# Optimization experiments

Hardware: AMD Instinct MI355X
Metric: run time of the kernel (lower is better)

## Reference

```python
import jax, jax.numpy as jnp
import numpy as np

NUM_NEG_PAIRS = 64
NUM_NEG_INDICES_FOR_LOSS = 16
B, C, H, W = 1, 64, 768, 768
HW = H * W


def setup_inputs() -> dict:
    key = jax.random.key(0)
    k1, k2, k3, k4 = jax.random.split(key, 4)
    feats1 = jax.random.normal(k1, (B, C, H, W), dtype=jnp.float32)
    feats2 = jax.random.normal(k2, (B, C, H, W), dtype=jnp.float32)
    positive_pairs = jax.random.randint(k3, (64, 2), 0, HW, dtype=jnp.int64 if jax.config.jax_enable_x64 else jnp.int32)
    negative_indices = jax.random.randint(k4, (NUM_NEG_PAIRS,), 0, HW, dtype=jnp.int64 if jax.config.jax_enable_x64 else jnp.int32)
    return {"feats1": feats1, "feats2": feats2,
            "positive_pairs": positive_pairs,
            "negative_indices": negative_indices}


def reference(feats1, feats2, positive_pairs, negative_indices):
    # feats1/feats2: [1, C, H, W] -> flatten to [C, HW] (matches .view(C, -1) with B=1)
    f1 = feats1.reshape(C, -1)
    f2 = feats2.reshape(C, -1)
    sel = f1[:, negative_indices]                      # [C, P]
    # squared L2 distance of each selected feature vs all HW locations of feats2
    # ||a-b||^2 = ||a||^2 + ||b||^2 - 2 a.b  (ReLU as in original; dist is nonneg)
    d = (jnp.sum(sel * sel, axis=0)[:, None]
         + jnp.sum(f2 * f2, axis=0)[None, :]
         - 2.0 * jnp.einsum('cp,cn->pn', sel, f2))     # [P, HW]
    d = jax.nn.relu(d)
    # NOTE: the original's mask-exclusion check compares FLOAT distance values
    # against an INT index mask (`dist[...].item() in mask`), which is never true
    # for continuous features, so the effective math is: take the K smallest
    # distances per negative, negate, and average.
    smallest = -jax.lax.top_k(-d, NUM_NEG_INDICES_FOR_LOSS)[0]   # [P, K] smallest dists
    negative_loss = jnp.mean(-smallest, axis=1)                   # [P]
    return jnp.mean(negative_loss)
```

## Files before the change

kernel.cpp:

```cpp
#include <hip/hip_runtime.h>
#include <cstdint>

#define CD 64
#define HWD 589824
#define K1_BLOCKS (HWD / 128)
#define FMAXV 3.402823466e+38f

#define AS1 __attribute__((address_space(1)))
#define AS3 __attribute__((address_space(3)))

typedef float f32x16 __attribute__((ext_vector_type(16)));
typedef short bf16x8 __attribute__((ext_vector_type(8)));

__device__ __forceinline__ short f2bf(float f) {
    unsigned u = __float_as_uint(f);
    u = u + 0x7FFFu + ((u >> 16) & 1u);
    return (short)(u >> 16);
}

__device__ __forceinline__ void ins4(float4& t, float x) {
    if (x < t.w) {
        if (x < t.z) { t.w = t.z;
            if (x < t.y) { t.z = t.y;
                if (x < t.x) { t.y = t.x; t.x = x; } else t.y = x;
            } else t.z = x;
        } else t.w = x;
    }
}

__global__ __launch_bounds__(64) void kA_pack(
    const float* __restrict__ f1, const int* __restrict__ nidx,
    short* __restrict__ sel_bf, float* __restrict__ sel2,
    unsigned* __restrict__ ticket)
{
    const int p = blockIdx.x, k = threadIdx.x;
    if (p == 0 && k == 0) *ticket = 0u;
    float v = f1[(long)k * HWD + nidx[p]];
    float s = v * v;
#pragma unroll
    for (int off = 32; off; off >>= 1) s += __shfl_xor(s, off);
    sel_bf[p * CD + k] = f2bf(v);
    if (k == 0) sel2[p] = s;
}

__global__ __launch_bounds__(256, 4) void k1_topk(
    const float* __restrict__ f2, const short* __restrict__ sel_bf,
    const float* __restrict__ sel2, float4* __restrict__ cells)
{
    __shared__ float lds[CD][128];
    __shared__ float4 lm[4][CD];
    const int tid = threadIdx.x;
    const int lane = tid & 63, wid = tid >> 6;
    const int l31 = lane & 31, lh = lane >> 5;
    const long n0 = (long)blockIdx.x * 128;

    {
        const int srow2 = lane >> 5;
        const int scol  = (lane & 31) * 4;
#pragma unroll
        for (int kk = 0; kk < 8; ++kk) {
            int k = wid * 16 + kk * 2;
            const float* gp = f2 + (long)(k + srow2) * HWD + n0 + scol;
            __builtin_amdgcn_global_load_lds((const AS1 void*)gp,
                                             (AS3 void*)&lds[k][0], 16, 0, 0);
        }
    }

    bf16x8 sf0[4], sf1[4];
#pragma unroll
    for (int ks = 0; ks < 4; ++ks) {
        sf0[ks] = *(const bf16x8*)(sel_bf + l31 * CD + 16 * ks + 8 * lh);
        sf1[ks] = *(const bf16x8*)(sel_bf + (l31 + 32) * CD + 16 * ks + 8 * lh);
    }
    const float sel20 = sel2[l31], sel21 = sel2[l31 + 32];

    __syncthreads();

    const int col = wid * 32 + l31;
    float fs = 0.f;
    f32x16 a0, a1;
#pragma unroll
    for (int i = 0; i < 16; ++i) { a0[i] = 0.f; a1[i] = 0.f; }
#pragma unroll
    for (int ks = 0; ks < 4; ++ks) {
        bf16x8 af;
#pragma unroll
        for (int j = 0; j < 8; ++j) {
            float v = lds[16 * ks + 8 * lh + j][col];
            fs += v * v;
            af[j] = f2bf(v);
        }
        a0 = __builtin_amdgcn_mfma_f32_32x32x16_bf16(af, sf0[ks], a0, 0, 0, 0);
        a1 = __builtin_amdgcn_mfma_f32_32x32x16_bf16(af, sf1[ks], a1, 0, 0, 0);
    }
    fs += __shfl_xor(fs, 32);

    float4 t = make_float4(FMAXV, FMAXV, FMAXV, FMAXV);
    float4 u = t;
#pragma unroll
    for (int i = 0; i < 16; ++i) {
        int r = (i & 3) + 8 * (i >> 2) + 4 * lh;
        float fr2 = __shfl(fs, r);
        ins4(t, fmaxf(sel20 + fr2 - 2.f * a0[i], 0.f));
        ins4(u, fmaxf(sel21 + fr2 - 2.f * a1[i], 0.f));
    }

    {
        float4 o;
        o.x = __shfl_xor(t.x, 32); o.y = __shfl_xor(t.y, 32);
        o.z = __shfl_xor(t.z, 32); o.w = __shfl_xor(t.w, 32);
        ins4(t, o.x); ins4(t, o.y); ins4(t, o.z); ins4(t, o.w);
        o.x = __shfl_xor(u.x, 32); o.y = __shfl_xor(u.y, 32);
        o.z = __shfl_xor(u.z, 32); o.w = __shfl_xor(u.w, 32);
        ins4(u, o.x); ins4(u, o.y); ins4(u, o.z); ins4(u, o.w);
    }
    if (lh == 0) { lm[wid][l31] = t; lm[wid][l31 + 32] = u; }
    __syncthreads();

    if (tid < CD) {
        float4 m  = lm[0][tid];
        float4 b1 = lm[1][tid], b2 = lm[2][tid], b3 = lm[3][tid];
        ins4(m, b1.x); ins4(m, b1.y); ins4(m, b1.z); ins4(m, b1.w);
        ins4(m, b2.x); ins4(m, b2.y); ins4(m, b2.z); ins4(m, b2.w);
        ins4(m, b3.x); ins4(m, b3.y); ins4(m, b3.z); ins4(m, b3.w);
        cells[(long)blockIdx.x * CD + tid] = m;
    }
}

__global__ __launch_bounds__(1024) void k2_sel(
    const float4* __restrict__ cells, float* __restrict__ partial,
    unsigned* __restrict__ ticket, float* __restrict__ out)
{
    const int p = blockIdx.x;
    const int tid = threadIdx.x;
    const int lane = tid & 63, wid = tid >> 6;
    __shared__ unsigned long long wmin[16];

    float4 b0 = cells[(long)(tid)        * CD + p];
    float4 b1 = cells[(long)(tid + 1024) * CD + p];
    float4 b2 = cells[(long)(tid + 2048) * CD + p];
    float4 b3 = cells[(long)(tid + 3072) * CD + p];
    float4 b4 = (tid < K1_BLOCKS - 4096)
                ? cells[(long)(tid + 4096) * CD + p]
                : make_float4(FMAXV, FMAXV, FMAXV, FMAXV);

    float4 t = make_float4(FMAXV, FMAXV, FMAXV, FMAXV);
    ins4(t, b0.x); ins4(t, b0.y); ins4(t, b0.z); ins4(t, b0.w);
    ins4(t, b1.x); ins4(t, b1.y); ins4(t, b1.z); ins4(t, b1.w);
    ins4(t, b2.x); ins4(t, b2.y); ins4(t, b2.z); ins4(t, b2.w);
    ins4(t, b3.x); ins4(t, b3.y); ins4(t, b3.z); ins4(t, b3.w);
    ins4(t, b4.x); ins4(t, b4.y); ins4(t, b4.z); ins4(t, b4.w);

    float sum = 0.f;
    for (int rd = 0; rd < 16; ++rd) {
        unsigned long long key =
            ((unsigned long long)__float_as_uint(t.x) << 32) | (unsigned)tid;
#pragma unroll
        for (int off = 32; off; off >>= 1) {
            unsigned long long o = __shfl_xor(key, off);
            if (o < key) key = o;
        }
        if (lane == 0) wmin[wid] = key;
        __syncthreads();
        unsigned long long gk = wmin[0];
#pragma unroll
        for (int w = 1; w < 16; ++w) if (wmin[w] < gk) gk = wmin[w];
        sum += __uint_as_float((unsigned)(gk >> 32));
        if ((unsigned)(gk & 0xFFFFFFFFu) == (unsigned)tid) {
            t.x = t.y; t.y = t.z; t.z = t.w; t.w = FMAXV;
        }
        __syncthreads();
    }

    if (tid == 0) {
        partial[p] = sum;
        __threadfence();
        unsigned tk = atomicAdd(ticket, 1u);
        if (tk == CD - 1) {
            __threadfence();
            float s = 0.f;
            const volatile float* vp = partial;
            for (int q = 0; q < CD; ++q) s += vp[q];
            out[0] = -s / 1024.0f;
        }
    }
}

extern "C" void kernel_launch(void* const* d_in, const int* in_sizes, int n_in,
                              void* d_out, int out_size, void* d_ws, size_t ws_size,
                              hipStream_t stream)
{
    const float* f1   = (const float*)d_in[0];
    const float* f2   = (const float*)d_in[1];
    const int*   nidx = (const int*)d_in[3];
    float* out = (float*)d_out;

    float4*   cells   = (float4*)d_ws;
    short*    sel_bf  = (short*)(cells + (long)K1_BLOCKS * CD);
    float*    sel2    = (float*)(sel_bf + CD * CD);
    float*    partial = sel2 + CD;
    unsigned* ticket  = (unsigned*)(partial + CD);

    kA_pack<<<CD,         64, 0, stream>>>(f1, nidx, sel_bf, sel2, ticket);
    k1_topk<<<K1_BLOCKS, 256, 0, stream>>>(f2, sel_bf, sel2, cells);
    k2_sel <<<CD,       1024, 0, stream>>>(cells, partial, ticket, out);
}
```

Measured before the change: 83.16 us.

## Make k1 persistent over four tiles with double-buffered async LDS loads

The top-k distance kernel now launches 1152 blocks, and each block processes four consecutive 128-column tiles. While the current tile runs its MFMA and insertion work, the next tile's global-to-LDS loads are already in flight in a second buffer, controlled by explicit waitcnt and barriers. This is meant to hide load latency and to amortise the per-block setup and selector register loads. In exchange, LDS use per block doubles, the occupancy hint drops to 2, and correctness depends on the hand-tuned vmcnt count matching the number of outstanding loads.

```diff
diff --git a/kernel.cpp b/kernel.cpp
--- a/kernel.cpp
+++ b/kernel.cpp
@@ -3,7 +3,9 @@
 
 #define CD 64
 #define HWD 589824
-#define K1_BLOCKS (HWD / 128)
+#define K1_GRID 1152
+#define T_PER 4
+#define K1_ROWS (K1_GRID * T_PER)
 #define FMAXV 3.402823466e+38f
 
 #define AS1 __attribute__((address_space(1)))
@@ -43,28 +45,28 @@
     if (k == 0) sel2[p] = s;
 }
 
-__global__ __launch_bounds__(256, 4) void k1_topk(
+__global__ __launch_bounds__(256, 2) void k1_topk(
     const float* __restrict__ f2, const short* __restrict__ sel_bf,
     const float* __restrict__ sel2, float4* __restrict__ cells)
 {
-    __shared__ float lds[CD][128];
+    __shared__ float lds[2][CD][128];
     __shared__ float4 lm[4][CD];
     const int tid = threadIdx.x;
     const int lane = tid & 63, wid = tid >> 6;
     const int l31 = lane & 31, lh = lane >> 5;
-    const long n0 = (long)blockIdx.x * 128;
-
-    {
-        const int srow2 = lane >> 5;
-        const int scol  = (lane & 31) * 4;
-#pragma unroll
-        for (int kk = 0; kk < 8; ++kk) {
-            int k = wid * 16 + kk * 2;
-            const float* gp = f2 + (long)(k + srow2) * HWD + n0 + scol;
-            __builtin_amdgcn_global_load_lds((const AS1 void*)gp,
-                                             (AS3 void*)&lds[k][0], 16, 0, 0);
-        }
-    }
+    const long nb = (long)blockIdx.x * (T_PER * 128);
+
+#define STAGE(buf, ncol0) do {                                              \
+        const int srow2_ = lane >> 5;                                       \
+        const int scol_  = (lane & 31) * 4;                                 \
+        _Pragma("unroll")                                                   \
+        for (int kk = 0; kk < 8; ++kk) {                                    \
+            int k_ = wid * 16 + kk * 2;                                     \
+            const float* gp_ = f2 + (long)(k_ + srow2_) * HWD + (ncol0) + scol_; \
+            __builtin_amdgcn_global_load_lds((const AS1 void*)gp_,          \
+                                             (AS3 void*)&lds[buf][k_][0], 16, 0, 0); \
+        }                                                                   \
+    } while (0)
 
     bf16x8 sf0[4], sf1[4];
 #pragma unroll
@@ -73,58 +75,77 @@
         sf1[ks] = *(const bf16x8*)(sel_bf + (l31 + 32) * CD + 16 * ks + 8 * lh);
     }
     const float sel20 = sel2[l31], sel21 = sel2[l31 + 32];
-
-    __syncthreads();
-
-    const int col = wid * 32 + l31;
-    float fs = 0.f;
-    f32x16 a0, a1;
-#pragma unroll
-    for (int i = 0; i < 16; ++i) { a0[i] = 0.f; a1[i] = 0.f; }
-#pragma unroll
-    for (int ks = 0; ks < 4; ++ks) {
-        bf16x8 af;
-#pragma unroll
-        for (int j = 0; j < 8; ++j) {
-            float v = lds[16 * ks + 8 * lh + j][col];
-            fs += v * v;
-            af[j] = f2bf(v);
-        }
-        a0 = __builtin_amdgcn_mfma_f32_32x32x16_bf16(af, sf0[ks], a0, 0, 0, 0);
-        a1 = __builtin_amdgcn_mfma_f32_32x32x16_bf16(af, sf1[ks], a1, 0, 0, 0);
-    }
-    fs += __shfl_xor(fs, 32);
-
-    float4 t = make_float4(FMAXV, FMAXV, FMAXV, FMAXV);
-    float4 u = t;
-#pragma unroll
-    for (int i = 0; i < 16; ++i) {
-        int r = (i & 3) + 8 * (i >> 2) + 4 * lh;
-        float fr2 = __shfl(fs, r);
-        ins4(t, fmaxf(sel20 + fr2 - 2.f * a0[i], 0.f));
-        ins4(u, fmaxf(sel21 + fr2 - 2.f * a1[i], 0.f));
-    }
-
-    {
-        float4 o;
-        o.x = __shfl_xor(t.x, 32); o.y = __shfl_xor(t.y, 32);
-        o.z = __shfl_xor(t.z, 32); o.w = __shfl_xor(t.w, 32);
-        ins4(t, o.x); ins4(t, o.y); ins4(t, o.z); ins4(t, o.w);
-        o.x = __shfl_xor(u.x, 32); o.y = __shfl_xor(u.y, 32);
-        o.z = __shfl_xor(u.z, 32); o.w = __shfl_xor(u.w, 32);
-        ins4(u, o.x); ins4(u, o.y); ins4(u, o.z); ins4(u, o.w);
-    }
-    if (lh == 0) { lm[wid][l31] = t; lm[wid][l31 + 32] = u; }
-    __syncthreads();
-
-    if (tid < CD) {
-        float4 m  = lm[0][tid];
-        float4 b1 = lm[1][tid], b2 = lm[2][tid], b3 = lm[3][tid];
-        ins4(m, b1.x); ins4(m, b1.y); ins4(m, b1.z); ins4(m, b1.w);
-        ins4(m, b2.x); ins4(m, b2.y); ins4(m, b2.z); ins4(m, b2.w);
-        ins4(m, b3.x); ins4(m, b3.y); ins4(m, b3.z); ins4(m, b3.w);
-        cells[(long)blockIdx.x * CD + tid] = m;
-    }
+    __builtin_amdgcn_sched_barrier(0);
+
+    STAGE(0, nb);
+    __builtin_amdgcn_sched_barrier(0);
+
+#pragma unroll
+    for (int t = 0; t < T_PER; ++t) {
+        if (t + 1 < T_PER) {
+            STAGE((t + 1) & 1, nb + (long)(t + 1) * 128);
+            __builtin_amdgcn_sched_barrier(0);
+            asm volatile("s_waitcnt vmcnt(8)" ::: "memory");
+        } else {
+            asm volatile("s_waitcnt vmcnt(0)" ::: "memory");
+        }
+        __builtin_amdgcn_sched_barrier(0);
+        __builtin_amdgcn_s_barrier();
+        __builtin_amdgcn_sched_barrier(0);
+
+        const int col = wid * 32 + l31;
+        float fs = 0.f;
+        f32x16 a0, a1;
+#pragma unroll
+        for (int i = 0; i < 16; ++i) { a0[i] = 0.f; a1[i] = 0.f; }
+#pragma unroll
+        for (int ks = 0; ks < 4; ++ks) {
+            bf16x8 af;
+#pragma unroll
+            for (int j = 0; j < 8; ++j) {
+                float v = lds[t & 1][16 * ks + 8 * lh + j][col];
+                fs += v * v;
+                af[j] = f2bf(v);
+            }
+            a0 = __builtin_amdgcn_mfma_f32_32x32x16_bf16(af, sf0[ks], a0, 0, 0, 0);
+            a1 = __builtin_amdgcn_mfma_f32_32x32x16_bf16(af, sf1[ks], a1, 0, 0, 0);
+        }
+        fs += __shfl_xor(fs, 32);
+
+        float4 tt = make_float4(FMAXV, FMAXV, FMAXV, FMAXV);
+        float4 uu = tt;
+#pragma unroll
+        for (int i = 0; i < 16; ++i) {
+            int r = (i & 3) + 8 * (i >> 2) + 4 * lh;
+            float fr2 = __shfl(fs, r);
+            ins4(tt, fmaxf(sel20 + fr2 - 2.f * a0[i], 0.f));
+            ins4(uu, fmaxf(sel21 + fr2 - 2.f * a1[i], 0.f));
+        }
+        {
+            float4 o;
+            o.x = __shfl_xor(tt.x, 32); o.y = __shfl_xor(tt.y, 32);
+            o.z = __shfl_xor(tt.z, 32); o.w = __shfl_xor(tt.w, 32);
+            ins4(tt, o.x); ins4(tt, o.y); ins4(tt, o.z); ins4(tt, o.w);
+            o.x = __shfl_xor(uu.x, 32); o.y = __shfl_xor(uu.y, 32);
+            o.z = __shfl_xor(uu.z, 32); o.w = __shfl_xor(uu.w, 32);
+            ins4(uu, o.x); ins4(uu, o.y); ins4(uu, o.z); ins4(uu, o.w);
+        }
+        if (lh == 0) { lm[wid][l31] = tt; lm[wid][l31 + 32] = uu; }
+        asm volatile("s_waitcnt lgkmcnt(0)" ::: "memory");
+        __builtin_amdgcn_sched_barrier(0);
+        __builtin_amdgcn_s_barrier();
+        __builtin_amdgcn_sched_barrier(0);
+
+        if (wid == (t & 3)) {
+            float4 m  = lm[0][lane];
+            float4 b1 = lm[1][lane], b2 = lm[2][lane], b3 = lm[3][lane];
+            ins4(m, b1.x); ins4(m, b1.y); ins4(m, b1.z); ins4(m, b1.w);
+            ins4(m, b2.x); ins4(m, b2.y); ins4(m, b2.z); ins4(m, b2.w);
+            ins4(m, b3.x); ins4(m, b3.y); ins4(m, b3.z); ins4(m, b3.w);
+            cells[(long)(blockIdx.x * T_PER + t) * CD + lane] = m;
+        }
+    }
+#undef STAGE
 }
 
 __global__ __launch_bounds__(1024) void k2_sel(
@@ -140,7 +161,7 @@
     float4 b1 = cells[(long)(tid + 1024) * CD + p];
     float4 b2 = cells[(long)(tid + 2048) * CD + p];
     float4 b3 = cells[(long)(tid + 3072) * CD + p];
-    float4 b4 = (tid < K1_BLOCKS - 4096)
+    float4 b4 = (tid < K1_ROWS - 4096)
                 ? cells[(long)(tid + 4096) * CD + p]
                 : make_float4(FMAXV, FMAXV, FMAXV, FMAXV);
 
@@ -196,12 +217,12 @@
     float* out = (float*)d_out;
 
     float4*   cells   = (float4*)d_ws;
-    short*    sel_bf  = (short*)(cells + (long)K1_BLOCKS * CD);
+    short*    sel_bf  = (short*)(cells + (long)K1_ROWS * CD);
     float*    sel2    = (float*)(sel_bf + CD * CD);
     float*    partial = sel2 + CD;
     unsigned* ticket  = (unsigned*)(partial + CD);
 
-    kA_pack<<<CD,         64, 0, stream>>>(f1, nidx, sel_bf, sel2, ticket);
-    k1_topk<<<K1_BLOCKS, 256, 0, stream>>>(f2, sel_bf, sel2, cells);
-    k2_sel <<<CD,       1024, 0, stream>>>(cells, partial, ticket, out);
-}
+    kA_pack<<<CD,        64, 0, stream>>>(f1, nidx, sel_bf, sel2, ticket);
+    k1_topk<<<K1_GRID,  256, 0, stream>>>(f2, sel_bf, sel2, cells);
+    k2_sel <<<CD,      1024, 0, stream>>>(cells, partial, ticket, out);
+}
```

New measurement: 108.8 us. 30.9% more time.

## Make each wave own four 32-column tiles with per-wave LDS and direct cell output

Applied to the files above, without the earlier changes.

Each wave now handles four consecutive 32-column tiles of feats2, loading every tile into its own per-wave LDS slice and keeping a running top-4 across tiles. This removes the block-level __syncthreads and the cross-wave LDS merge, and amortizes the selection-fragment loads over more work. The grid shrinks to 1152 blocks, and each wave writes its own cell row, so the cell count stays at 4608 for the second kernel. The trade-off is that each tile load is followed by a full vmcnt wait with no prefetch, so memory latency is serialized within a wave. Fewer blocks may also leave fewer waves in flight to hide that latency.

```diff
diff --git a/kernel.cpp b/kernel.cpp
--- a/kernel.cpp
+++ b/kernel.cpp
@@ -3,7 +3,9 @@
 
 #define CD 64
 #define HWD 589824
-#define K1_BLOCKS (HWD / 128)
+#define K1_GRID 1152
+#define T_PER 4
+#define K1_ROWS (K1_GRID * 4)
 #define FMAXV 3.402823466e+38f
 
 #define AS1 __attribute__((address_space(1)))
@@ -47,24 +49,12 @@
     const float* __restrict__ f2, const short* __restrict__ sel_bf,
     const float* __restrict__ sel2, float4* __restrict__ cells)
 {
-    __shared__ float lds[CD][128];
-    __shared__ float4 lm[4][CD];
+    __shared__ float lds[4][CD][32];
     const int tid = threadIdx.x;
     const int lane = tid & 63, wid = tid >> 6;
     const int l31 = lane & 31, lh = lane >> 5;
-    const long n0 = (long)blockIdx.x * 128;
-
-    {
-        const int srow2 = lane >> 5;
-        const int scol  = (lane & 31) * 4;
-#pragma unroll
-        for (int kk = 0; kk < 8; ++kk) {
-            int k = wid * 16 + kk * 2;
-            const float* gp = f2 + (long)(k + srow2) * HWD + n0 + scol;
-            __builtin_amdgcn_global_load_lds((const AS1 void*)gp,
-                                             (AS3 void*)&lds[k][0], 16, 0, 0);
-        }
-    }
+    const int gw = blockIdx.x * 4 + wid;
+    const long nb = (long)gw * (T_PER * 32);
 
     bf16x8 sf0[4], sf1[4];
 #pragma unroll
@@ -74,35 +64,52 @@
     }
     const float sel20 = sel2[l31], sel21 = sel2[l31 + 32];
 
-    __syncthreads();
-
-    const int col = wid * 32 + l31;
-    float fs = 0.f;
-    f32x16 a0, a1;
-#pragma unroll
-    for (int i = 0; i < 16; ++i) { a0[i] = 0.f; a1[i] = 0.f; }
-#pragma unroll
-    for (int ks = 0; ks < 4; ++ks) {
-        bf16x8 af;
-#pragma unroll
-        for (int j = 0; j < 8; ++j) {
-            float v = lds[16 * ks + 8 * lh + j][col];
-            fs += v * v;
-            af[j] = f2bf(v);
-        }
-        a0 = __builtin_amdgcn_mfma_f32_32x32x16_bf16(af, sf0[ks], a0, 0, 0, 0);
-        a1 = __builtin_amdgcn_mfma_f32_32x32x16_bf16(af, sf1[ks], a1, 0, 0, 0);
-    }
-    fs += __shfl_xor(fs, 32);
+    const int srow = lane >> 3;
+    const int scol = (lane & 7) * 4;
 
     float4 t = make_float4(FMAXV, FMAXV, FMAXV, FMAXV);
     float4 u = t;
-#pragma unroll
-    for (int i = 0; i < 16; ++i) {
-        int r = (i & 3) + 8 * (i >> 2) + 4 * lh;
-        float fr2 = __shfl(fs, r);
-        ins4(t, fmaxf(sel20 + fr2 - 2.f * a0[i], 0.f));
-        ins4(u, fmaxf(sel21 + fr2 - 2.f * a1[i], 0.f));
+
+#pragma unroll
+    for (int tt = 0; tt < T_PER; ++tt) {
+        const long n0 = nb + (long)tt * 32;
+
+#pragma unroll
+        for (int kk = 0; kk < 8; ++kk) {
+            const float* gp = f2 + (long)(8 * kk + srow) * HWD + n0 + scol;
+            __builtin_amdgcn_global_load_lds((const AS1 void*)gp,
+                                             (AS3 void*)&lds[wid][8 * kk][0], 16, 0, 0);
+        }
+        asm volatile("s_waitcnt vmcnt(0)" ::: "memory");
+        __builtin_amdgcn_sched_barrier(0);
+
+        float fs = 0.f;
+        f32x16 a0, a1;
+#pragma unroll
+        for (int i = 0; i < 16; ++i) { a0[i] = 0.f; a1[i] = 0.f; }
+#pragma unroll
+        for (int ks = 0; ks < 4; ++ks) {
+            bf16x8 af;
+#pragma unroll
+            for (int j = 0; j < 8; ++j) {
+                float v = lds[wid][16 * ks + 8 * lh + j][l31];
+                fs += v * v;
+                af[j] = f2bf(v);
+            }
+            a0 = __builtin_amdgcn_mfma_f32_32x32x16_bf16(af, sf0[ks], a0, 0, 0, 0);
+            a1 = __builtin_amdgcn_mfma_f32_32x32x16_bf16(af, sf1[ks], a1, 0, 0, 0);
+        }
+        fs += __shfl_xor(fs, 32);
+
+#pragma unroll
+        for (int i = 0; i < 16; ++i) {
+            int r = (i & 3) + 8 * (i >> 2) + 4 * lh;
+            float fr2 = __shfl(fs, r);
+            ins4(t, fmaxf(sel20 + fr2 - 2.f * a0[i], 0.f));
+            ins4(u, fmaxf(sel21 + fr2 - 2.f * a1[i], 0.f));
+        }
+        asm volatile("s_waitcnt lgkmcnt(0)" ::: "memory");
+        __builtin_amdgcn_sched_barrier(0);
     }
 
     {
@@ -114,16 +121,9 @@
         o.z = __shfl_xor(u.z, 32); o.w = __shfl_xor(u.w, 32);
         ins4(u, o.x); ins4(u, o.y); ins4(u, o.z); ins4(u, o.w);
     }
-    if (lh == 0) { lm[wid][l31] = t; lm[wid][l31 + 32] = u; }
-    __syncthreads();
-
-    if (tid < CD) {
-        float4 m  = lm[0][tid];
-        float4 b1 = lm[1][tid], b2 = lm[2][tid], b3 = lm[3][tid];
-        ins4(m, b1.x); ins4(m, b1.y); ins4(m, b1.z); ins4(m, b1.w);
-        ins4(m, b2.x); ins4(m, b2.y); ins4(m, b2.z); ins4(m, b2.w);
-        ins4(m, b3.x); ins4(m, b3.y); ins4(m, b3.z); ins4(m, b3.w);
-        cells[(long)blockIdx.x * CD + tid] = m;
+    if (lh == 0) {
+        cells[(long)gw * CD + l31]      = t;
+        cells[(long)gw * CD + l31 + 32] = u;
     }
 }
 
@@ -140,7 +140,7 @@
     float4 b1 = cells[(long)(tid + 1024) * CD + p];
     float4 b2 = cells[(long)(tid + 2048) * CD + p];
     float4 b3 = cells[(long)(tid + 3072) * CD + p];
-    float4 b4 = (tid < K1_BLOCKS - 4096)
+    float4 b4 = (tid < K1_ROWS - 4096)
                 ? cells[(long)(tid + 4096) * CD + p]
                 : make_float4(FMAXV, FMAXV, FMAXV, FMAXV);
 
@@ -196,12 +196,12 @@
     float* out = (float*)d_out;
 
     float4*   cells   = (float4*)d_ws;
-    short*    sel_bf  = (short*)(cells + (long)K1_BLOCKS * CD);
+    short*    sel_bf  = (short*)(cells + (long)K1_ROWS * CD);
     float*    sel2    = (float*)(sel_bf + CD * CD);
     float*    partial = sel2 + CD;
     unsigned* ticket  = (unsigned*)(partial + CD);
 
-    kA_pack<<<CD,         64, 0, stream>>>(f1, nidx, sel_bf, sel2, ticket);
-    k1_topk<<<K1_BLOCKS, 256, 0, stream>>>(f2, sel_bf, sel2, cells);
-    k2_sel <<<CD,       1024, 0, stream>>>(cells, partial, ticket, out);
-}
+    kA_pack<<<CD,        64, 0, stream>>>(f1, nidx, sel_bf, sel2, ticket);
+    k1_topk<<<K1_GRID,  256, 0, stream>>>(f2, sel_bf, sel2, cells);
+    k2_sel <<<CD,      1024, 0, stream>>>(cells, partial, ticket, out);
+}
```

Result: no change. 84.18 us (+1.2%).
